# Kernel tuning notes

Hardware: AMD Instinct MI355X
Metric: run time of the kernel (lower is better)

The kernel has to match this reference:

```python
import jax, jax.numpy as jnp
import numpy as np

B, N, D, U = 8, 4096, 128, 1024


def setup_inputs() -> dict:
    key = jax.random.key(0)
    kx, kw = jax.random.split(key)
    x = jax.random.normal(kx, (B, N, D), dtype=jnp.float32)
    # learned kernel, shape (dims, units) as in build()
    w = jax.random.normal(kw, (D, U), dtype=jnp.float32)
    return {"x": x, "w": w}


def reference(x, w):
    # Squared Euclidean distance from every point x[b,n,:] to every prototype
    # column w[:,u]: sum_d (x[b,n,d] - w[d,u])^2.
    # work is a single GEMM instead of materializing a [B,N,D,U] tensor.
    x2 = jnp.sum(x * x, axis=-1, keepdims=True)        # [B, N, 1]
    w2 = jnp.sum(w * w, axis=0)                        # [U]
    xw = jnp.einsum("bnd,du->bnu", x, w)               # [B, N, U]
    a = x2 + w2 - 2.0 * xw                             # [B, N, U]
    # inverted=False, activation=None -> return raw squared distances
    return a
```

## Files before the change

kernel.cpp:

```cpp
#include <hip/hip_runtime.h>

#define M_TOT 32768
#define K_DIM 128
#define U_TOT 1024

typedef short s16x8 __attribute__((ext_vector_type(8)));
typedef float f32x4 __attribute__((ext_vector_type(4)));

__device__ inline unsigned int f2bf(float f) {
    union { float f; unsigned int u; } v; v.f = f;
    unsigned int r = v.u + 0x7FFFu + ((v.u >> 16) & 1u);
    return r >> 16;
}

__global__ __launch_bounds__(256) void prep_kernel(
    const float* __restrict__ x, const float* __restrict__ w,
    unsigned int* __restrict__ xb, unsigned int* __restrict__ wt,
    float* __restrict__ x2, float* __restrict__ w2)
{
    const int lane = threadIdx.x & 63;
    const int gw = (blockIdx.x << 2) + (threadIdx.x >> 6);
    if (gw < M_TOT) {
        const float2 v = ((const float2*)(x + (size_t)gw * K_DIM))[lane];
        float s = v.x * v.x + v.y * v.y;
        #pragma unroll
        for (int off = 32; off; off >>= 1) s += __shfl_xor(s, off);
        xb[gw * 64 + lane] = f2bf(v.x) | (f2bf(v.y) << 16);
        if (lane == 0) x2[gw] = s;
    } else if (gw < M_TOT + U_TOT) {
        const int u = gw - M_TOT;
        const float a = w[(size_t)(2 * lane) * U_TOT + u];
        const float b = w[(size_t)(2 * lane + 1) * U_TOT + u];
        float s = a * a + b * b;
        #pragma unroll
        for (int off = 32; off; off >>= 1) s += __shfl_xor(s, off);
        wt[u * 64 + lane] = f2bf(a) | (f2bf(b) << 16);
        if (lane == 0) w2[u] = s;
    }
}

__global__ __launch_bounds__(256) void gemm_kernel(
    const unsigned short* __restrict__ xb, const unsigned short* __restrict__ wt,
    const float* __restrict__ x2, const float* __restrict__ w2,
    float* __restrict__ out)
{
    const int tid = threadIdx.x;
    const int wv = tid >> 6;
    const int lane = tid & 63;
    const int col = lane & 15;
    const int quad = lane >> 4;
    const int m0 = (int)(blockIdx.x >> 3) * 128;
    const int u0 = (int)(blockIdx.x & 7) * 128;
    const int wm = (wv & 1) * 64;
    const int wn = (wv >> 1) * 64;

    const unsigned short* arow = xb + (size_t)(m0 + wm + col) * K_DIM;
    const unsigned short* brow = wt + (size_t)(u0 + wn + col) * K_DIM;

    f32x4 acc[4][4] = {};

    #pragma unroll 1
    for (int kc = 0; kc < 4; ++kc) {
        const int ko = kc * 32 + quad * 8;
        s16x8 af[4], bf[4];
        #pragma unroll
        for (int t = 0; t < 4; ++t) {
            af[t] = *(const s16x8*)(arow + t * 16 * K_DIM + ko);
            bf[t] = *(const s16x8*)(brow + t * 16 * K_DIM + ko);
        }
        #pragma unroll
        for (int a = 0; a < 4; ++a)
            #pragma unroll
            for (int b = 0; b < 4; ++b)
                acc[a][b] = __builtin_amdgcn_mfma_f32_16x16x32_bf16(bf[b], af[a], acc[a][b], 0, 0, 0);
    }

    float xs[4];
    #pragma unroll
    for (int a = 0; a < 4; ++a) xs[a] = x2[m0 + wm + a * 16 + col];
    float4 ws4[4];
    #pragma unroll
    for (int b = 0; b < 4; ++b) ws4[b] = *(const float4*)&w2[u0 + wn + b * 16 + quad * 4];

    #pragma unroll
    for (int a = 0; a < 4; ++a) {
        const size_t mrow = (size_t)(m0 + wm + a * 16 + col) * U_TOT;
        #pragma unroll
        for (int b = 0; b < 4; ++b) {
            const int ub = u0 + wn + b * 16 + quad * 4;
            float4 o;
            o.x = xs[a] + ws4[b].x - 2.0f * acc[a][b][0];
            o.y = xs[a] + ws4[b].y - 2.0f * acc[a][b][1];
            o.z = xs[a] + ws4[b].z - 2.0f * acc[a][b][2];
            o.w = xs[a] + ws4[b].w - 2.0f * acc[a][b][3];
            *(float4*)&out[mrow + ub] = o;
        }
    }
}

__global__ __launch_bounds__(256) void fallback_kernel(
    const float* __restrict__ x, const float* __restrict__ w,
    float* __restrict__ out)
{
    __shared__ float xrow[K_DIM];
    const int m = blockIdx.x;
    const int tid = threadIdx.x;
    if (tid < K_DIM) xrow[tid] = x[(size_t)m * K_DIM + tid];
    __syncthreads();
    float x2 = 0.f;
    #pragma unroll
    for (int k = 0; k < K_DIM; ++k) x2 += xrow[k] * xrow[k];
    #pragma unroll
    for (int uu = 0; uu < 4; ++uu) {
        const int u = uu * 256 + tid;
        float dot = 0.f, w2 = 0.f;
        for (int k = 0; k < K_DIM; ++k) {
            const float wv = w[(size_t)k * U_TOT + u];
            dot += xrow[k] * wv;
            w2 += wv * wv;
        }
        out[(size_t)m * U_TOT + u] = x2 + w2 - 2.0f * dot;
    }
}

extern "C" void kernel_launch(void* const* d_in, const int* in_sizes, int n_in,
                              void* d_out, int out_size, void* d_ws, size_t ws_size,
                              hipStream_t stream) {
    const float* x = (const float*)d_in[0];
    const float* w = (const float*)d_in[1];
    float* out = (float*)d_out;

    const size_t need = (size_t)M_TOT * K_DIM * 2 + (size_t)U_TOT * K_DIM * 2
                      + (size_t)M_TOT * 4 + (size_t)U_TOT * 4;
    if (ws_size < need) {
        fallback_kernel<<<M_TOT, 256, 0, stream>>>(x, w, out);
        return;
    }

    unsigned short* xb = (unsigned short*)d_ws;
    unsigned short* wt = xb + (size_t)M_TOT * K_DIM;
    float* x2 = (float*)(wt + (size_t)U_TOT * K_DIM);
    float* w2 = x2 + M_TOT;

    prep_kernel<<<(M_TOT + U_TOT) / 4, 256, 0, stream>>>(x, w, (unsigned int*)xb,
                                                         (unsigned int*)wt, x2, w2);
    gemm_kernel<<<(M_TOT / 128) * (U_TOT / 128), 256, 0, stream>>>(xb, wt, x2, w2, out);
}
```

Before: 182.6 us.

## Fuse x bf16 conversion and row norms into the GEMM kernel

The x preprocessing pass is removed. The GEMM now loads fp32 x directly, converts it to bf16 in registers and accumulates the squared row norms with a cross-quad shuffle reduction. Only w is still preprocessed in a separate small kernel. This avoids writing and rereading a bf16 copy of x plus a separate norm array. In exchange, each tile loads twice the bytes for the A operand and repeats the conversion once per column block.

Result: slower. 194.7 us (+6.6%).

```diff
diff --git a/kernel.cpp b/kernel.cpp
--- a/kernel.cpp
+++ b/kernel.cpp
@@ -13,36 +13,23 @@
     return r >> 16;
 }
 
-__global__ __launch_bounds__(256) void prep_kernel(
-    const float* __restrict__ x, const float* __restrict__ w,
-    unsigned int* __restrict__ xb, unsigned int* __restrict__ wt,
-    float* __restrict__ x2, float* __restrict__ w2)
+__global__ __launch_bounds__(256) void prep_w(
+    const float* __restrict__ w, unsigned int* __restrict__ wt, float* __restrict__ w2)
 {
     const int lane = threadIdx.x & 63;
-    const int gw = (blockIdx.x << 2) + (threadIdx.x >> 6);
-    if (gw < M_TOT) {
-        const float2 v = ((const float2*)(x + (size_t)gw * K_DIM))[lane];
-        float s = v.x * v.x + v.y * v.y;
-        #pragma unroll
-        for (int off = 32; off; off >>= 1) s += __shfl_xor(s, off);
-        xb[gw * 64 + lane] = f2bf(v.x) | (f2bf(v.y) << 16);
-        if (lane == 0) x2[gw] = s;
-    } else if (gw < M_TOT + U_TOT) {
-        const int u = gw - M_TOT;
-        const float a = w[(size_t)(2 * lane) * U_TOT + u];
-        const float b = w[(size_t)(2 * lane + 1) * U_TOT + u];
-        float s = a * a + b * b;
-        #pragma unroll
-        for (int off = 32; off; off >>= 1) s += __shfl_xor(s, off);
-        wt[u * 64 + lane] = f2bf(a) | (f2bf(b) << 16);
-        if (lane == 0) w2[u] = s;
-    }
+    const int u = (blockIdx.x << 2) + (threadIdx.x >> 6);
+    const float a = w[(size_t)(2 * lane) * U_TOT + u];
+    const float b = w[(size_t)(2 * lane + 1) * U_TOT + u];
+    float s = a * a + b * b;
+    #pragma unroll
+    for (int off = 32; off; off >>= 1) s += __shfl_xor(s, off);
+    wt[u * 64 + lane] = f2bf(a) | (f2bf(b) << 16);
+    if (lane == 0) w2[u] = s;
 }
 
 __global__ __launch_bounds__(256) void gemm_kernel(
-    const unsigned short* __restrict__ xb, const unsigned short* __restrict__ wt,
-    const float* __restrict__ x2, const float* __restrict__ w2,
-    float* __restrict__ out)
+    const float* __restrict__ x, const unsigned short* __restrict__ wt,
+    const float* __restrict__ w2, float* __restrict__ out)
 {
     const int tid = threadIdx.x;
     const int wv = tid >> 6;
@@ -54,19 +41,29 @@
     const int wm = (wv & 1) * 64;
     const int wn = (wv >> 1) * 64;
 
-    const unsigned short* arow = xb + (size_t)(m0 + wm + col) * K_DIM;
-    const unsigned short* brow = wt + (size_t)(u0 + wn + col) * K_DIM;
+    const float* xrow = x + (size_t)(m0 + wm + col) * K_DIM + quad * 8;
+    const unsigned short* brow = wt + (size_t)(u0 + wn + col) * K_DIM + quad * 8;
 
     f32x4 acc[4][4] = {};
+    float x2p[4] = {0.f, 0.f, 0.f, 0.f};
 
     #pragma unroll 1
     for (int kc = 0; kc < 4; ++kc) {
-        const int ko = kc * 32 + quad * 8;
         s16x8 af[4], bf[4];
         #pragma unroll
         for (int t = 0; t < 4; ++t) {
-            af[t] = *(const s16x8*)(arow + t * 16 * K_DIM + ko);
-            bf[t] = *(const s16x8*)(brow + t * 16 * K_DIM + ko);
+            const float* ap = xrow + (size_t)t * 16 * K_DIM + kc * 32;
+            const float4 lo = *(const float4*)(ap);
+            const float4 hi = *(const float4*)(ap + 4);
+            x2p[t] += lo.x * lo.x + lo.y * lo.y + lo.z * lo.z + lo.w * lo.w
+                    + hi.x * hi.x + hi.y * hi.y + hi.z * hi.z + hi.w * hi.w;
+            union { unsigned int u[4]; s16x8 v; } pk;
+            pk.u[0] = f2bf(lo.x) | (f2bf(lo.y) << 16);
+            pk.u[1] = f2bf(lo.z) | (f2bf(lo.w) << 16);
+            pk.u[2] = f2bf(hi.x) | (f2bf(hi.y) << 16);
+            pk.u[3] = f2bf(hi.z) | (f2bf(hi.w) << 16);
+            af[t] = pk.v;
+            bf[t] = *(const s16x8*)(brow + (size_t)t * 16 * K_DIM + kc * 32);
         }
         #pragma unroll
         for (int a = 0; a < 4; ++a)
@@ -77,7 +74,13 @@
 
     float xs[4];
     #pragma unroll
-    for (int a = 0; a < 4; ++a) xs[a] = x2[m0 + wm + a * 16 + col];
+    for (int t = 0; t < 4; ++t) {
+        float s = x2p[t];
+        s += __shfl_xor(s, 16);
+        s += __shfl_xor(s, 32);
+        xs[t] = s;
+    }
+
     float4 ws4[4];
     #pragma unroll
     for (int b = 0; b < 4; ++b) ws4[b] = *(const float4*)&w2[u0 + wn + b * 16 + quad * 4];
@@ -130,19 +133,15 @@
     const float* w = (const float*)d_in[1];
     float* out = (float*)d_out;
 
-    const size_t need = (size_t)M_TOT * K_DIM * 2 + (size_t)U_TOT * K_DIM * 2
-                      + (size_t)M_TOT * 4 + (size_t)U_TOT * 4;
+    const size_t need = (size_t)U_TOT * K_DIM * 2 + (size_t)U_TOT * 4;
     if (ws_size < need) {
         fallback_kernel<<<M_TOT, 256, 0, stream>>>(x, w, out);
         return;
     }
 
-    unsigned short* xb = (unsigned short*)d_ws;
-    unsigned short* wt = xb + (size_t)M_TOT * K_DIM;
-    float* x2 = (float*)(wt + (size_t)U_TOT * K_DIM);
-    float* w2 = x2 + M_TOT;
+    unsigned short* wt = (unsigned short*)d_ws;
+    float* w2 = (float*)(wt + (size_t)U_TOT * K_DIM);
 
-    prep_kernel<<<(M_TOT + U_TOT) / 4, 256, 0, stream>>>(x, w, (unsigned int*)xb,
-                                                         (unsigned int*)wt, x2, w2);
-    gemm_kernel<<<(M_TOT / 128) * (U_TOT / 128), 256, 0, stream>>>(xb, wt, x2, w2, out);
+    prep_w<<<U_TOT / 4, 256, 0, stream>>>(w, (unsigned int*)wt, w2);
+    gemm_kernel<<<(M_TOT / 128) * (U_TOT / 128), 256, 0, stream>>>(x, wt, w2, out);
 }
```
